# Performance work log

Measured on AMD Instinct MI355X. Metric: run time of the kernel, lower is better.

Reference implementation:

```python
import jax, jax.numpy as jnp
import numpy as np

B, C, E = 2, 128, 60000

def conv1(x, W, b):
    # pointwise conv1d: x [B,Cin,E], W [Cout,Cin], b [Cout] -> [B,Cout,E]
    return jnp.einsum('oc,bce->boe', W, x) + b[None, :, None]

def mesh_conv(x, gi, W, b):
    # MeshCNN GeMM conv: x [B,C,E], gi [B,E,4] neighbor edge ids, W [Cout,Cin,5], b [Cout]
    f = jax.vmap(lambda xb, ib: xb[:, ib])(x, gi)  # [B,C,E,4] neighbor gather
    f1, f2, f3, f4 = f[..., 0], f[..., 1], f[..., 2], f[..., 3]
    # symmetric features: [e, a+c, b+d, |a-c|, |b-d|]
    G = jnp.stack([x, f1 + f3, f2 + f4, jnp.abs(f1 - f3), jnp.abs(f2 - f4)], axis=-1)  # [B,C,E,5]
    return jnp.einsum('bces,ocs->boe', G, W) + b[None, :, None]


def setup_inputs() -> dict:
    key = jax.random.key(0)
    ks = jax.random.split(key, 16)
    s = 0.05
    return {
        'x_0': jax.random.normal(ks[0], (B, C, E), jnp.float32),
        'x_1': jax.random.normal(ks[1], (B, C, E), jnp.float32),
        'gemm': jax.random.randint(ks[2], (B, E, 4), 0, E, jnp.int32),
        'Wa_local': jax.random.normal(ks[3], (C, C), jnp.float32) * s,
        'ba_local': jax.random.normal(ks[4], (C,), jnp.float32) * s,
        'Wb_local': jax.random.normal(ks[5], (C, C), jnp.float32) * s,
        'bb_local': jax.random.normal(ks[6], (C,), jnp.float32) * s,
        'Wa_tri': jax.random.normal(ks[7], (C, C, 5), jnp.float32) * s,
        'ba_tri': jax.random.normal(ks[8], (C,), jnp.float32) * s,
        'Wb_tri': jax.random.normal(ks[9], (C, C, 5), jnp.float32) * s,
        'bb_tri': jax.random.normal(ks[10], (C,), jnp.float32) * s,
        'Wa_fuse': jax.random.normal(ks[11], (3, 2 * C), jnp.float32) * s,
        'ba_fuse': jax.random.normal(ks[12], (3,), jnp.float32) * s,
        'Wb_fuse': jax.random.normal(ks[13], (3, 2 * C), jnp.float32) * s,
        'bb_fuse': jax.random.normal(ks[14], (3,), jnp.float32) * s,
    }


def reference(x_0, x_1, gemm, Wa_local, ba_local, Wb_local, bb_local,
              Wa_tri, ba_tri, Wb_tri, bb_tri,
              Wa_fuse, ba_fuse, Wb_fuse, bb_fuse):
    a_local = conv1(x_0, Wa_local, ba_local)              # [B,C,E]
    a_tri = mesh_conv(x_0, gemm, Wa_tri, ba_tri)          # [B,C,E]
    x_a_two = jnp.concatenate([a_local, a_tri], axis=1)   # [B,2C,E]
    b_local = conv1(x_1, Wb_local, bb_local)
    b_tri = mesh_conv(x_1, gemm, Wb_tri, bb_tri)
    x_b_two = jnp.concatenate([b_local, b_tri], axis=1)
    x_a_w = conv1(x_a_two, Wa_fuse, ba_fuse)[:, None]     # [B,1,3,E]
    x_b_w = conv1(x_b_two, Wb_fuse, bb_fuse)[:, None]     # [B,1,3,E]
    return x_a_w + x_b_w
```

## Files before the change

### kernel.cpp

```cpp
#include <hip/hip_runtime.h>
#include <hip/hip_bf16.h>
#include <cstdint>

#define B_ 2
#define C_ 128
#define E_ 60000

typedef unsigned int uint32_;
typedef unsigned short ushort_;
typedef float v2f __attribute__((ext_vector_type(2)));

__device__ __forceinline__ v2f bp2(uint32_ v) {
    v2f r;
    r.x = __uint_as_float(v << 16);
    r.y = __uint_as_float(v & 0xffff0000u);
    return r;
}

__device__ __forceinline__ v2f vabs2(v2f a) {
    v2f r; r.x = fabsf(a.x); r.y = fabsf(a.y); return r;
}

__device__ __forceinline__ ushort_ f2b(float f) {
    union { float f; uint32_ u; } x; x.f = f;
    uint32_ u = x.u + 0x7fffu + ((x.u >> 16) & 1u);
    return (ushort_)(u >> 16);
}

__device__ __forceinline__ float swz_add(float v, const int pat) {
    switch (pat) {
    case 1:  return v + __int_as_float(__builtin_amdgcn_ds_swizzle(__float_as_int(v), 0x041F));
    case 2:  return v + __int_as_float(__builtin_amdgcn_ds_swizzle(__float_as_int(v), 0x081F));
    case 4:  return v + __int_as_float(__builtin_amdgcn_ds_swizzle(__float_as_int(v), 0x101F));
    case 8:  return v + __int_as_float(__builtin_amdgcn_ds_swizzle(__float_as_int(v), 0x201F));
    default: return v + __int_as_float(__builtin_amdgcn_ds_swizzle(__float_as_int(v), 0x401F));
    }
}

__global__ __launch_bounds__(256) void fuse_weights_kernel(
    const float* __restrict__ Wa_local, const float* __restrict__ ba_local,
    const float* __restrict__ Wb_local, const float* __restrict__ bb_local,
    const float* __restrict__ Wa_tri,  const float* __restrict__ ba_tri,
    const float* __restrict__ Wb_tri,  const float* __restrict__ bb_tri,
    const float* __restrict__ Wa_fuse, const float* __restrict__ ba_fuse,
    const float* __restrict__ Wb_fuse, const float* __restrict__ bb_fuse,
    float* __restrict__ Vw, float* __restrict__ cst)
{
    const int lane = threadIdx.x & 63;
    if (blockIdx.x < 15) {
        const int wid   = blockIdx.x * 4 + (threadIdx.x >> 6);
        const int pj    = wid / 10;
        const int chunk = wid % 10;
        const int p = pj / 3, j = pj % 3;
        const int f = chunk * 64 + lane;
        const float* Wf = p ? Wb_fuse : Wa_fuse;
        const float* Wt = p ? Wb_tri  : Wa_tri;
        const float* Wl = p ? Wb_local : Wa_local;
        float a0 = 0.f, a1 = 0.f, a2 = 0.f, a3 = 0.f;
        for (int o = 0; o < C_; o += 4) {
            a0 += Wf[j * 256 + 128 + o]     * Wt[(o)     * 640 + f];
            a1 += Wf[j * 256 + 128 + o + 1] * Wt[(o + 1) * 640 + f];
            a2 += Wf[j * 256 + 128 + o + 2] * Wt[(o + 2) * 640 + f];
            a3 += Wf[j * 256 + 128 + o + 3] * Wt[(o + 3) * 640 + f];
        }
        float acc = (a0 + a1) + (a2 + a3);
        const int s = f % 5, c = f / 5;
        if (s == 0) {
            float b0 = 0.f, b1 = 0.f, b2 = 0.f, b3 = 0.f;
            for (int o = 0; o < C_; o += 4) {
                b0 += Wf[j * 256 + o]     * Wl[(o)     * C_ + c];
                b1 += Wf[j * 256 + o + 1] * Wl[(o + 1) * C_ + c];
                b2 += Wf[j * 256 + o + 2] * Wl[(o + 2) * C_ + c];
                b3 += Wf[j * 256 + o + 3] * Wl[(o + 3) * C_ + c];
            }
            acc += (b0 + b1) + (b2 + b3);
        }
        Vw[(pj * 5 + s) * C_ + c] = acc;
    } else {
        if (threadIdx.x < 3) {
            int j = threadIdx.x;
            float acc = ba_fuse[j] + bb_fuse[j];
            for (int o = 0; o < C_; ++o) {
                acc += Wa_fuse[j * 256 + o]       * ba_local[o]
                     + Wa_fuse[j * 256 + 128 + o] * ba_tri[o]
                     + Wb_fuse[j * 256 + o]       * bb_local[o]
                     + Wb_fuse[j * 256 + 128 + o] * bb_tri[o];
            }
            cst[j] = acc;
        }
    }
}

__global__ __launch_bounds__(256) void transpose_bf16_kernel(
    const float* __restrict__ x0, const float* __restrict__ x1,
    ushort_* __restrict__ x0t, ushort_* __restrict__ x1t)
{
    __shared__ float tile[32][65];
    const int which = blockIdx.z >> 1;
    const int b     = blockIdx.z & 1;
    const float* src = (which ? x1 : x0) + (size_t)b * C_ * E_;
    ushort_*     dst = (which ? x1t : x0t) + (size_t)b * E_ * C_;
    const int e0 = blockIdx.x * 32;
    const int c0 = blockIdx.y * 64;
    const int t  = threadIdx.x;
    {
        const int c  = t >> 2;
        const int e8 = (t & 3) * 8;
        const float* p = src + (size_t)(c0 + c) * E_ + e0 + e8;
        float4 v0 = *(const float4*)p;
        float4 v1 = *(const float4*)(p + 4);
        tile[e8 + 0][c] = v0.x; tile[e8 + 1][c] = v0.y;
        tile[e8 + 2][c] = v0.z; tile[e8 + 3][c] = v0.w;
        tile[e8 + 4][c] = v1.x; tile[e8 + 5][c] = v1.y;
        tile[e8 + 6][c] = v1.z; tile[e8 + 7][c] = v1.w;
    }
    __syncthreads();
    {
        const int e  = t >> 3;
        const int c8 = (t & 7) * 8;
        const float* r = &tile[e][c8];
        uint32_ w0 = (uint32_)f2b(r[0]) | ((uint32_)f2b(r[1]) << 16);
        uint32_ w1 = (uint32_)f2b(r[2]) | ((uint32_)f2b(r[3]) << 16);
        uint32_ w2 = (uint32_)f2b(r[4]) | ((uint32_)f2b(r[5]) << 16);
        uint32_ w3 = (uint32_)f2b(r[6]) | ((uint32_)f2b(r[7]) << 16);
        uint4 w; w.x = w0; w.y = w1; w.z = w2; w.w = w3;
        *(uint4*)(dst + (size_t)(e0 + e) * C_ + c0 + c8) = w;
    }
}

__global__ __launch_bounds__(256, 4) void mesh_fused_kernel(
    const uint32_* __restrict__ x0t, const uint32_* __restrict__ x1t,
    const int* __restrict__ gemm, const float* __restrict__ Vw,
    const float* __restrict__ cst, float* __restrict__ out)
{
    const int lane = threadIdx.x & 63;
    const int wv   = threadIdx.x >> 6;
    const int gw   = blockIdx.x * 4 + wv;
    const int nw   = gridDim.x * 4;

    v2f w[2][3][5];
#pragma unroll
    for (int p = 0; p < 2; ++p)
#pragma unroll
        for (int j = 0; j < 3; ++j)
#pragma unroll
            for (int s = 0; s < 5; ++s)
                w[p][j][s] = *(const v2f*)(Vw + (((p * 3 + j) * 5 + s) << 7) + lane * 2);

    const int  jj     = lane >> 4;
    const bool is0    = (jj == 0), is1 = (jj == 1);
    const bool writer = ((lane & 15) == 0) && (jj < 3);
    const float cj    = is0 ? cst[0] : (is1 ? cst[1] : cst[2]);
    float* obase      = out + (size_t)(jj < 3 ? jj : 2) * E_;

    const int4* g4 = (const int4*)gemm;
    const int npair = (B_ * E_) / 2;

    int4 giA = make_int4(0, 0, 0, 0), giB = giA;
    if (gw < npair) { giA = g4[2 * gw]; giB = g4[2 * gw + 1]; }

    for (int pair = gw; pair < npair; pair += nw) {
        const int nxt = pair + nw;
        const int4 gA = giA, gB = giB;
        if (nxt < npair) { giA = g4[2 * nxt]; giB = g4[2 * nxt + 1]; }

        const int e0 = 2 * pair;
        const int b  = (e0 >= E_) ? 1 : 0;
        const int e  = e0 - (b ? E_ : 0);
        const uint32_* xa = x0t + (size_t)b * (E_ * 64);
        const uint32_* xb = x1t + (size_t)b * (E_ * 64);

        const uint32_ sA = ((uint32_)e << 6) + lane;
        const uint32_ sB = sA + 64;
        const uint32_ oA1 = ((uint32_)gA.x << 6) + lane;
        const uint32_ oA2 = ((uint32_)gA.y << 6) + lane;
        const uint32_ oA3 = ((uint32_)gA.z << 6) + lane;
        const uint32_ oA4 = ((uint32_)gA.w << 6) + lane;
        const uint32_ oB1 = ((uint32_)gB.x << 6) + lane;
        const uint32_ oB2 = ((uint32_)gB.y << 6) + lane;
        const uint32_ oB3 = ((uint32_)gB.z << 6) + lane;
        const uint32_ oB4 = ((uint32_)gB.w << 6) + lane;

        const uint32_ A0 = xa[sA],  A1 = xa[oA1], A2 = xa[oA2], A3 = xa[oA3], A4 = xa[oA4];
        const uint32_ C0 = xb[sA],  C1 = xb[oA1], C2 = xb[oA2], C3 = xb[oA3], C4 = xb[oA4];
        const uint32_ D0 = xa[sB],  D1 = xa[oB1], D2 = xa[oB2], D3 = xa[oB3], D4 = xa[oB4];
        const uint32_ F0 = xb[sB],  F1 = xb[oB1], F2 = xb[oB2], F3 = xb[oB3], F4 = xb[oB4];

        float rA0, rA1, rA2;
        {
            v2f a0 = bp2(A0), a1 = bp2(A1), a2 = bp2(A2), a3 = bp2(A3), a4 = bp2(A4);
            v2f b0 = bp2(C0), b1 = bp2(C1), b2 = bp2(C2), b3 = bp2(C3), b4 = bp2(C4);
            v2f sa1 = a1 + a3, sa2 = a2 + a4;
            v2f da1 = vabs2(a1 - a3), da2 = vabs2(a2 - a4);
            v2f sb1 = b1 + b3, sb2 = b2 + b4;
            v2f db1 = vabs2(b1 - b3), db2 = vabs2(b2 - b4);
            v2f t0 = w[0][0][0] * a0, t1 = w[0][1][0] * a0, t2 = w[0][2][0] * a0;
            t0 += w[0][0][1] * sa1; t1 += w[0][1][1] * sa1; t2 += w[0][2][1] * sa1;
            t0 += w[0][0][2] * sa2; t1 += w[0][1][2] * sa2; t2 += w[0][2][2] * sa2;
            t0 += w[0][0][3] * da1; t1 += w[0][1][3] * da1; t2 += w[0][2][3] * da1;
            t0 += w[0][0][4] * da2; t1 += w[0][1][4] * da2; t2 += w[0][2][4] * da2;
            t0 += w[1][0][0] * b0;  t1 += w[1][1][0] * b0;  t2 += w[1][2][0] * b0;
            t0 += w[1][0][1] * sb1; t1 += w[1][1][1] * sb1; t2 += w[1][2][1] * sb1;
            t0 += w[1][0][2] * sb2; t1 += w[1][1][2] * sb2; t2 += w[1][2][2] * sb2;
            t0 += w[1][0][3] * db1; t1 += w[1][1][3] * db1; t2 += w[1][2][3] * db1;
            t0 += w[1][0][4] * db2; t1 += w[1][1][4] * db2; t2 += w[1][2][4] * db2;
            rA0 = t0.x + t0.y; rA1 = t1.x + t1.y; rA2 = t2.x + t2.y;
        }
        float rB0, rB1, rB2;
        {
            v2f a0 = bp2(D0), a1 = bp2(D1), a2 = bp2(D2), a3 = bp2(D3), a4 = bp2(D4);
            v2f b0 = bp2(F0), b1 = bp2(F1), b2 = bp2(F2), b3 = bp2(F3), b4 = bp2(F4);
            v2f sa1 = a1 + a3, sa2 = a2 + a4;
            v2f da1 = vabs2(a1 - a3), da2 = vabs2(a2 - a4);
            v2f sb1 = b1 + b3, sb2 = b2 + b4;
            v2f db1 = vabs2(b1 - b3), db2 = vabs2(b2 - b4);
            v2f t0 = w[0][0][0] * a0, t1 = w[0][1][0] * a0, t2 = w[0][2][0] * a0;
            t0 += w[0][0][1] * sa1; t1 += w[0][1][1] * sa1; t2 += w[0][2][1] * sa1;
            t0 += w[0][0][2] * sa2; t1 += w[0][1][2] * sa2; t2 += w[0][2][2] * sa2;
            t0 += w[0][0][3] * da1; t1 += w[0][1][3] * da1; t2 += w[0][2][3] * da1;
            t0 += w[0][0][4] * da2; t1 += w[0][1][4] * da2; t2 += w[0][2][4] * da2;
            t0 += w[1][0][0] * b0;  t1 += w[1][1][0] * b0;  t2 += w[1][2][0] * b0;
            t0 += w[1][0][1] * sb1; t1 += w[1][1][1] * sb1; t2 += w[1][2][1] * sb1;
            t0 += w[1][0][2] * sb2; t1 += w[1][1][2] * sb2; t2 += w[1][2][2] * sb2;
            t0 += w[1][0][3] * db1; t1 += w[1][1][3] * db1; t2 += w[1][2][3] * db1;
            t0 += w[1][0][4] * db2; t1 += w[1][1][4] * db2; t2 += w[1][2][4] * db2;
            rB0 = t0.x + t0.y; rB1 = t1.x + t1.y; rB2 = t2.x + t2.y;
        }

        rA0 = swz_add(rA0, 16); rB0 = swz_add(rB0, 16);
        rA1 = swz_add(rA1, 16); rB1 = swz_add(rB1, 16);
        rA2 = swz_add(rA2, 16); rB2 = swz_add(rB2, 16);
        rA0 += __shfl_xor(rA0, 32, 64); rB0 += __shfl_xor(rB0, 32, 64);
        rA1 += __shfl_xor(rA1, 32, 64); rB1 += __shfl_xor(rB1, 32, 64);
        rA2 += __shfl_xor(rA2, 32, 64); rB2 += __shfl_xor(rB2, 32, 64);

        float vA = is0 ? rA0 : (is1 ? rA1 : rA2);
        float vB = is0 ? rB0 : (is1 ? rB1 : rB2);
        vA = swz_add(vA, 1); vB = swz_add(vB, 1);
        vA = swz_add(vA, 2); vB = swz_add(vB, 2);
        vA = swz_add(vA, 4); vB = swz_add(vB, 4);
        vA = swz_add(vA, 8); vB = swz_add(vB, 8);

        if (writer) {
            float2 st; st.x = vA + cj; st.y = vB + cj;
            *(float2*)(obase + (b ? 3 * E_ : 0) + e) = st;
        }
    }
}

extern "C" void kernel_launch(void* const* d_in, const int* in_sizes, int n_in,
                              void* d_out, int out_size, void* d_ws, size_t ws_size,
                              hipStream_t stream) {
    const float* x0       = (const float*)d_in[0];
    const float* x1       = (const float*)d_in[1];
    const int*   gemm     = (const int*)d_in[2];
    const float* Wa_local = (const float*)d_in[3];
    const float* ba_local = (const float*)d_in[4];
    const float* Wb_local = (const float*)d_in[5];
    const float* bb_local = (const float*)d_in[6];
    const float* Wa_tri   = (const float*)d_in[7];
    const float* ba_tri   = (const float*)d_in[8];
    const float* Wb_tri   = (const float*)d_in[9];
    const float* bb_tri   = (const float*)d_in[10];
    const float* Wa_fuse  = (const float*)d_in[11];
    const float* ba_fuse  = (const float*)d_in[12];
    const float* Wb_fuse  = (const float*)d_in[13];
    const float* bb_fuse  = (const float*)d_in[14];
    float* out = (float*)d_out;

    ushort_* x0t = (ushort_*)d_ws;
    ushort_* x1t = x0t + (size_t)B_ * E_ * C_;
    float*   Vw  = (float*)(x1t + (size_t)B_ * E_ * C_);
    float*   cst = Vw + 2 * 3 * 5 * C_;

    hipLaunchKernelGGL(fuse_weights_kernel, dim3(16), dim3(256), 0, stream,
                       Wa_local, ba_local, Wb_local, bb_local,
                       Wa_tri, ba_tri, Wb_tri, bb_tri,
                       Wa_fuse, ba_fuse, Wb_fuse, bb_fuse, Vw, cst);

    hipLaunchKernelGGL(transpose_bf16_kernel, dim3(E_ / 32, C_ / 64, 2 * B_),
                       dim3(256), 0, stream, x0, x1, x0t, x1t);

    hipLaunchKernelGGL(mesh_fused_kernel, dim3(2048), dim3(256), 0, stream,
                       (const uint32_*)x0t, (const uint32_*)x1t, gemm, Vw, cst, out);
}
```

Measured before the change: 227.7 us.

## Interleave x0 and x1 bf16 rows into one buffer for paired gathers

The transpose kernel now writes x0 and x1 into a single interleaved bf16 buffer, where each uint2 holds a channel pair from x0 next to the same pair from x1. The mesh kernel then gathers each neighbor edge with one 8-byte load instead of two separate 4-byte loads from two arrays. This halves the number of gather instructions and puts both inputs for an edge in the same cache lines, aiming to improve random-access efficiency. The transpose kernel uses twice the LDS per block, and its grid shrinks to one block per (b, tile) for both tensors.

After: 227.7 us. Within noise of the previous version (+0.0%).

```diff
diff --git a/kernel.cpp b/kernel.cpp
--- a/kernel.cpp
+++ b/kernel.cpp
@@ -25,6 +25,10 @@
     union { float f; uint32_ u; } x; x.f = f;
     uint32_ u = x.u + 0x7fffu + ((x.u >> 16) & 1u);
     return (ushort_)(u >> 16);
+}
+
+__device__ __forceinline__ uint32_ packb(float lo, float hi) {
+    return (uint32_)f2b(lo) | ((uint32_)f2b(hi) << 16);
 }
 
 __device__ __forceinline__ float swz_add(float v, const int pat) {
@@ -91,47 +95,57 @@
     }
 }
 
-__global__ __launch_bounds__(256) void transpose_bf16_kernel(
+__global__ __launch_bounds__(256) void transpose_interleave_kernel(
     const float* __restrict__ x0, const float* __restrict__ x1,
-    ushort_* __restrict__ x0t, ushort_* __restrict__ x1t)
+    uint32_* __restrict__ y)
 {
-    __shared__ float tile[32][65];
-    const int which = blockIdx.z >> 1;
-    const int b     = blockIdx.z & 1;
-    const float* src = (which ? x1 : x0) + (size_t)b * C_ * E_;
-    ushort_*     dst = (which ? x1t : x0t) + (size_t)b * E_ * C_;
+    __shared__ float tA[32][65];
+    __shared__ float tB[32][65];
+    const int b  = blockIdx.z;
     const int e0 = blockIdx.x * 32;
     const int c0 = blockIdx.y * 64;
-    const int t  = threadIdx.x;
+    const float* s0 = x0 + (size_t)b * C_ * E_;
+    const float* s1 = x1 + (size_t)b * C_ * E_;
+    const int t = threadIdx.x;
     {
         const int c  = t >> 2;
         const int e8 = (t & 3) * 8;
-        const float* p = src + (size_t)(c0 + c) * E_ + e0 + e8;
-        float4 v0 = *(const float4*)p;
-        float4 v1 = *(const float4*)(p + 4);
-        tile[e8 + 0][c] = v0.x; tile[e8 + 1][c] = v0.y;
-        tile[e8 + 2][c] = v0.z; tile[e8 + 3][c] = v0.w;
-        tile[e8 + 4][c] = v1.x; tile[e8 + 5][c] = v1.y;
-        tile[e8 + 6][c] = v1.z; tile[e8 + 7][c] = v1.w;
+        const float* p0 = s0 + (size_t)(c0 + c) * E_ + e0 + e8;
+        const float* p1 = s1 + (size_t)(c0 + c) * E_ + e0 + e8;
+        float4 u0 = *(const float4*)p0;
+        float4 u1 = *(const float4*)(p0 + 4);
+        float4 v0 = *(const float4*)p1;
+        float4 v1 = *(const float4*)(p1 + 4);
+        tA[e8 + 0][c] = u0.x; tA[e8 + 1][c] = u0.y;
+        tA[e8 + 2][c] = u0.z; tA[e8 + 3][c] = u0.w;
+        tA[e8 + 4][c] = u1.x; tA[e8 + 5][c] = u1.y;
+        tA[e8 + 6][c] = u1.z; tA[e8 + 7][c] = u1.w;
+        tB[e8 + 0][c] = v0.x; tB[e8 + 1][c] = v0.y;
+        tB[e8 + 2][c] = v0.z; tB[e8 + 3][c] = v0.w;
+        tB[e8 + 4][c] = v1.x; tB[e8 + 5][c] = v1.y;
+        tB[e8 + 6][c] = v1.z; tB[e8 + 7][c] = v1.w;
     }
     __syncthreads();
     {
         const int e  = t >> 3;
         const int c8 = (t & 7) * 8;
-        const float* r = &tile[e][c8];
-        uint32_ w0 = (uint32_)f2b(r[0]) | ((uint32_)f2b(r[1]) << 16);
-        uint32_ w1 = (uint32_)f2b(r[2]) | ((uint32_)f2b(r[3]) << 16);
-        uint32_ w2 = (uint32_)f2b(r[4]) | ((uint32_)f2b(r[5]) << 16);
-        uint32_ w3 = (uint32_)f2b(r[6]) | ((uint32_)f2b(r[7]) << 16);
-        uint4 w; w.x = w0; w.y = w1; w.z = w2; w.w = w3;
-        *(uint4*)(dst + (size_t)(e0 + e) * C_ + c0 + c8) = w;
+        const float* ra = &tA[e][c8];
+        const float* rb = &tB[e][c8];
+        uint4 w0, w1;
+        w0.x = packb(ra[0], ra[1]); w0.y = packb(rb[0], rb[1]);
+        w0.z = packb(ra[2], ra[3]); w0.w = packb(rb[2], rb[3]);
+        w1.x = packb(ra[4], ra[5]); w1.y = packb(rb[4], rb[5]);
+        w1.z = packb(ra[6], ra[7]); w1.w = packb(rb[6], rb[7]);
+        uint32_* drow = y + (((size_t)(b * E_ + e0 + e)) << 7) + c0 + c8;
+        *(uint4*)(drow)     = w0;
+        *(uint4*)(drow + 4) = w1;
     }
 }
 
 __global__ __launch_bounds__(256, 4) void mesh_fused_kernel(
-    const uint32_* __restrict__ x0t, const uint32_* __restrict__ x1t,
-    const int* __restrict__ gemm, const float* __restrict__ Vw,
-    const float* __restrict__ cst, float* __restrict__ out)
+    const uint2* __restrict__ y, const int* __restrict__ gemm,
+    const float* __restrict__ Vw, const float* __restrict__ cst,
+    float* __restrict__ out)
 {
     const int lane = threadIdx.x & 63;
     const int wv   = threadIdx.x >> 6;
@@ -167,11 +181,10 @@
         const int e0 = 2 * pair;
         const int b  = (e0 >= E_) ? 1 : 0;
         const int e  = e0 - (b ? E_ : 0);
-        const uint32_* xa = x0t + (size_t)b * (E_ * 64);
-        const uint32_* xb = x1t + (size_t)b * (E_ * 64);
-
-        const uint32_ sA = ((uint32_)e << 6) + lane;
-        const uint32_ sB = sA + 64;
+        const uint2* Y = y + (size_t)b * (E_ * 64);
+
+        const uint32_ sA  = ((uint32_)e    << 6) + lane;
+        const uint32_ sB  = sA + 64;
         const uint32_ oA1 = ((uint32_)gA.x << 6) + lane;
         const uint32_ oA2 = ((uint32_)gA.y << 6) + lane;
         const uint32_ oA3 = ((uint32_)gA.z << 6) + lane;
@@ -181,15 +194,17 @@
         const uint32_ oB3 = ((uint32_)gB.z << 6) + lane;
         const uint32_ oB4 = ((uint32_)gB.w << 6) + lane;
 
-        const uint32_ A0 = xa[sA],  A1 = xa[oA1], A2 = xa[oA2], A3 = xa[oA3], A4 = xa[oA4];
-        const uint32_ C0 = xb[sA],  C1 = xb[oA1], C2 = xb[oA2], C3 = xb[oA3], C4 = xb[oA4];
-        const uint32_ D0 = xa[sB],  D1 = xa[oB1], D2 = xa[oB2], D3 = xa[oB3], D4 = xa[oB4];
-        const uint32_ F0 = xb[sB],  F1 = xb[oB1], F2 = xb[oB2], F3 = xb[oB3], F4 = xb[oB4];
+        const uint2 PA0 = Y[sA],  PA1 = Y[oA1], PA2 = Y[oA2],
+                    PA3 = Y[oA3], PA4 = Y[oA4];
+        const uint2 PB0 = Y[sB],  PB1 = Y[oB1], PB2 = Y[oB2],
+                    PB3 = Y[oB3], PB4 = Y[oB4];
 
         float rA0, rA1, rA2;
         {
-            v2f a0 = bp2(A0), a1 = bp2(A1), a2 = bp2(A2), a3 = bp2(A3), a4 = bp2(A4);
-            v2f b0 = bp2(C0), b1 = bp2(C1), b2 = bp2(C2), b3 = bp2(C3), b4 = bp2(C4);
+            v2f a0 = bp2(PA0.x), a1 = bp2(PA1.x), a2 = bp2(PA2.x),
+                a3 = bp2(PA3.x), a4 = bp2(PA4.x);
+            v2f b0 = bp2(PA0.y), b1 = bp2(PA1.y), b2 = bp2(PA2.y),
+                b3 = bp2(PA3.y), b4 = bp2(PA4.y);
             v2f sa1 = a1 + a3, sa2 = a2 + a4;
             v2f da1 = vabs2(a1 - a3), da2 = vabs2(a2 - a4);
             v2f sb1 = b1 + b3, sb2 = b2 + b4;
@@ -208,8 +223,10 @@
         }
         float rB0, rB1, rB2;
         {
-            v2f a0 = bp2(D0), a1 = bp2(D1), a2 = bp2(D2), a3 = bp2(D3), a4 = bp2(D4);
-            v2f b0 = bp2(F0), b1 = bp2(F1), b2 = bp2(F2), b3 = bp2(F3), b4 = bp2(F4);
+            v2f a0 = bp2(PB0.x), a1 = bp2(PB1.x), a2 = bp2(PB2.x),
+                a3 = bp2(PB3.x), a4 = bp2(PB4.x);
+            v2f b0 = bp2(PB0.y), b1 = bp2(PB1.y), b2 = bp2(PB2.y),
+                b3 = bp2(PB3.y), b4 = bp2(PB4.y);
             v2f sa1 = a1 + a3, sa2 = a2 + a4;
             v2f da1 = vabs2(a1 - a3), da2 = vabs2(a2 - a4);
             v2f sb1 = b1 + b3, sb2 = b2 + b4;
@@ -268,9 +285,8 @@
     const float* bb_fuse  = (const float*)d_in[14];
     float* out = (float*)d_out;
 
-    ushort_* x0t = (ushort_*)d_ws;
-    ushort_* x1t = x0t + (size_t)B_ * E_ * C_;
-    float*   Vw  = (float*)(x1t + (size_t)B_ * E_ * C_);
+    uint32_* y   = (uint32_*)d_ws;
+    float*   Vw  = (float*)(y + (size_t)B_ * E_ * 128);
     float*   cst = Vw + 2 * 3 * 5 * C_;
 
     hipLaunchKernelGGL(fuse_weights_kernel, dim3(16), dim3(256), 0, stream,
@@ -278,9 +294,9 @@
                        Wa_tri, ba_tri, Wb_tri, bb_tri,
                        Wa_fuse, ba_fuse, Wb_fuse, bb_fuse, Vw, cst);
 
-    hipLaunchKernelGGL(transpose_bf16_kernel, dim3(E_ / 32, C_ / 64, 2 * B_),
-                       dim3(256), 0, stream, x0, x1, x0t, x1t);
+    hipLaunchKernelGGL(transpose_interleave_kernel, dim3(E_ / 32, C_ / 64, B_),
+                       dim3(256), 0, stream, x0, x1, y);
 
     hipLaunchKernelGGL(mesh_fused_kernel, dim3(2048), dim3(256), 0, stream,
-                       (const uint32_*)x0t, (const uint32_*)x1t, gemm, Vw, cst, out);
-}
+                       (const uint2*)y, gemm, Vw, cst, out);
+}
```

## Interleave x0/x1 bf16 layout and fold self-edge term into transpose kernel

Applied to the files above, without the earlier changes.

The transpose kernel now processes x0 and x1 together, writing one interleaved bf16 buffer so each neighbor gather fetches both inputs with a single 8-byte load. It also computes the self-edge (s=0) contribution, including the local conv, as a per-edge partial sum and writes it to a psum buffer. The mesh kernel therefore drops the self-edge loads and their FMAs, and adds psum at the write. In exchange the transpose kernel does more work and carries extra register pressure, and the design adds a small intermediate buffer plus one extra read per output.

Measured after the change: 250.0 us. 1.1x slower.

```diff
diff --git a/kernel.cpp b/kernel.cpp
--- a/kernel.cpp
+++ b/kernel.cpp
@@ -25,6 +25,10 @@
     union { float f; uint32_ u; } x; x.f = f;
     uint32_ u = x.u + 0x7fffu + ((x.u >> 16) & 1u);
     return (ushort_)(u >> 16);
+}
+
+__device__ __forceinline__ uint32_ packb(float lo, float hi) {
+    return (uint32_)f2b(lo) | ((uint32_)f2b(hi) << 16);
 }
 
 __device__ __forceinline__ float swz_add(float v, const int pat) {
@@ -44,7 +48,7 @@
     const float* __restrict__ Wb_tri,  const float* __restrict__ bb_tri,
     const float* __restrict__ Wa_fuse, const float* __restrict__ ba_fuse,
     const float* __restrict__ Wb_fuse, const float* __restrict__ bb_fuse,
-    float* __restrict__ Vw, float* __restrict__ cst)
+    float* __restrict__ Vw, float* __restrict__ Vs, float* __restrict__ cst)
 {
     const int lane = threadIdx.x & 63;
     if (blockIdx.x < 15) {
@@ -74,8 +78,10 @@
                 b3 += Wf[j * 256 + o + 3] * Wl[(o + 3) * C_ + c];
             }
             acc += (b0 + b1) + (b2 + b3);
+            Vs[pj * C_ + c] = acc;
+        } else {
+            Vw[(pj * 5 + s) * C_ + c] = acc;
         }
-        Vw[(pj * 5 + s) * C_ + c] = acc;
     } else {
         if (threadIdx.x < 3) {
             int j = threadIdx.x;
@@ -91,67 +97,131 @@
     }
 }
 
-__global__ __launch_bounds__(256) void transpose_bf16_kernel(
+__global__ __launch_bounds__(256) void transpose_fused_kernel(
     const float* __restrict__ x0, const float* __restrict__ x1,
-    ushort_* __restrict__ x0t, ushort_* __restrict__ x1t)
+    uint32_* __restrict__ y, const float* __restrict__ Vs,
+    float* __restrict__ psum)
 {
-    __shared__ float tile[32][65];
-    const int which = blockIdx.z >> 1;
-    const int b     = blockIdx.z & 1;
-    const float* src = (which ? x1 : x0) + (size_t)b * C_ * E_;
-    ushort_*     dst = (which ? x1t : x0t) + (size_t)b * E_ * C_;
-    const int e0 = blockIdx.x * 32;
-    const int c0 = blockIdx.y * 64;
-    const int t  = threadIdx.x;
+    __shared__ float tile[32][131];
+    const int b   = blockIdx.y;
+    const int e0  = blockIdx.x * 32;
+    const int t   = threadIdx.x;
+    const int c   = t >> 1;
+    const int eh  = (t & 1) * 16;
+    const int e   = t >> 3;
+    const int k16 = (t & 7) * 16;
+
+    const float* s0 = x0 + (size_t)b * C_ * E_ + (size_t)c * E_ + e0 + eh;
+    const float* s1 = x1 + (size_t)b * C_ * E_ + (size_t)c * E_ + e0 + eh;
+
+    float ra[16], rb[16];
+
     {
-        const int c  = t >> 2;
-        const int e8 = (t & 3) * 8;
-        const float* p = src + (size_t)(c0 + c) * E_ + e0 + e8;
-        float4 v0 = *(const float4*)p;
-        float4 v1 = *(const float4*)(p + 4);
-        tile[e8 + 0][c] = v0.x; tile[e8 + 1][c] = v0.y;
-        tile[e8 + 2][c] = v0.z; tile[e8 + 3][c] = v0.w;
-        tile[e8 + 4][c] = v1.x; tile[e8 + 5][c] = v1.y;
-        tile[e8 + 6][c] = v1.z; tile[e8 + 7][c] = v1.w;
-    }
+        float4 v0 = *(const float4*)(s0);
+        float4 v1 = *(const float4*)(s0 + 4);
+        float4 v2 = *(const float4*)(s0 + 8);
+        float4 v3 = *(const float4*)(s0 + 12);
+        tile[eh + 0][c] = v0.x;  tile[eh + 1][c] = v0.y;
+        tile[eh + 2][c] = v0.z;  tile[eh + 3][c] = v0.w;
+        tile[eh + 4][c] = v1.x;  tile[eh + 5][c] = v1.y;
+        tile[eh + 6][c] = v1.z;  tile[eh + 7][c] = v1.w;
+        tile[eh + 8][c] = v2.x;  tile[eh + 9][c] = v2.y;
+        tile[eh + 10][c] = v2.z; tile[eh + 11][c] = v2.w;
+        tile[eh + 12][c] = v3.x; tile[eh + 13][c] = v3.y;
+        tile[eh + 14][c] = v3.z; tile[eh + 15][c] = v3.w;
+    }
+    __syncthreads();
+#pragma unroll
+    for (int i = 0; i < 16; ++i) ra[i] = tile[e][k16 + i];
     __syncthreads();
     {
-        const int e  = t >> 3;
-        const int c8 = (t & 7) * 8;
-        const float* r = &tile[e][c8];
-        uint32_ w0 = (uint32_)f2b(r[0]) | ((uint32_)f2b(r[1]) << 16);
-        uint32_ w1 = (uint32_)f2b(r[2]) | ((uint32_)f2b(r[3]) << 16);
-        uint32_ w2 = (uint32_)f2b(r[4]) | ((uint32_)f2b(r[5]) << 16);
-        uint32_ w3 = (uint32_)f2b(r[6]) | ((uint32_)f2b(r[7]) << 16);
-        uint4 w; w.x = w0; w.y = w1; w.z = w2; w.w = w3;
-        *(uint4*)(dst + (size_t)(e0 + e) * C_ + c0 + c8) = w;
-    }
-}
+        float4 v0 = *(const float4*)(s1);
+        float4 v1 = *(const float4*)(s1 + 4);
+        float4 v2 = *(const float4*)(s1 + 8);
+        float4 v3 = *(const float4*)(s1 + 12);
+        tile[eh + 0][c] = v0.x;  tile[eh + 1][c] = v0.y;
+        tile[eh + 2][c] = v0.z;  tile[eh + 3][c] = v0.w;
+        tile[eh + 4][c] = v1.x;  tile[eh + 5][c] = v1.y;
+        tile[eh + 6][c] = v1.z;  tile[eh + 7][c] = v1.w;
+        tile[eh + 8][c] = v2.x;  tile[eh + 9][c] = v2.y;
+        tile[eh + 10][c] = v2.z; tile[eh + 11][c] = v2.w;
+        tile[eh + 12][c] = v3.x; tile[eh + 13][c] = v3.y;
+        tile[eh + 14][c] = v3.z; tile[eh + 15][c] = v3.w;
+    }
+    __syncthreads();
+#pragma unroll
+    for (int i = 0; i < 16; ++i) rb[i] = tile[e][k16 + i];
+
+    uint32_* drow = y + (((size_t)(b * E_ + e0 + e)) << 7) + k16;
+#pragma unroll
+    for (int m = 0; m < 4; ++m) {
+        uint4 w_;
+        w_.x = packb(ra[4 * m],     ra[4 * m + 1]);
+        w_.y = packb(rb[4 * m],     rb[4 * m + 1]);
+        w_.z = packb(ra[4 * m + 2], ra[4 * m + 3]);
+        w_.w = packb(rb[4 * m + 2], rb[4 * m + 3]);
+        *(uint4*)(drow + 4 * m) = w_;
+    }
+
+    float p0 = 0.f, p1 = 0.f, p2 = 0.f;
+#pragma unroll
+    for (int i = 0; i < 16; ++i) {
+        const float va = ra[i], vb = rb[i];
+        p0 += Vs[0 * C_ + k16 + i] * va + Vs[3 * C_ + k16 + i] * vb;
+        p1 += Vs[1 * C_ + k16 + i] * va + Vs[4 * C_ + k16 + i] * vb;
+        p2 += Vs[2 * C_ + k16 + i] * va + Vs[5 * C_ + k16 + i] * vb;
+    }
+    p0 = swz_add(p0, 1); p0 = swz_add(p0, 2); p0 = swz_add(p0, 4);
+    p1 = swz_add(p1, 1); p1 = swz_add(p1, 2); p1 = swz_add(p1, 4);
+    p2 = swz_add(p2, 1); p2 = swz_add(p2, 2); p2 = swz_add(p2, 4);
+    const int m = t & 7;
+    if (m < 3) {
+        float v = (m == 0) ? p0 : ((m == 1) ? p1 : p2);
+        psum[((size_t)b * 3 + m) * E_ + e0 + e] = v;
+    }
+}
+
+#define LDW(p, j, s) (*(const v2f*)(Vw + ((((p) * 3 + (j)) * 5 + (s)) << 7) + (lane << 1)))
+
+#define EDGE_DOT(P1,P2,P3,P4, R0,R1,R2) do {                                  \
+    v2f a1 = bp2(P1.x), a2 = bp2(P2.x), a3 = bp2(P3.x), a4 = bp2(P4.x);       \
+    v2f b1 = bp2(P1.y), b2 = bp2(P2.y), b3 = bp2(P3.y), b4 = bp2(P4.y);       \
+    v2f sa1 = a1 + a3, sa2 = a2 + a4;                                         \
+    v2f da1 = vabs2(a1 - a3), da2 = vabs2(a2 - a4);                           \
+    v2f sb1 = b1 + b3, sb2 = b2 + b4;                                         \
+    v2f db1 = vabs2(b1 - b3), db2 = vabs2(b2 - b4);                           \
+    v2f t0 = w001 * sa1 + w002 * sa2 + w003 * da1 + w004 * da2                \
+           + w101 * sb1 + w102 * sb2 + w103 * db1 + w104 * db2;               \
+    v2f t1 = w011 * sa1 + w012 * sa2 + w013 * da1 + w014 * da2                \
+           + w111 * sb1 + w112 * sb2 + w113 * db1 + w114 * db2;               \
+    v2f t2 = w021 * sa1 + w022 * sa2 + w023 * da1 + w024 * da2                \
+           + w121 * sb1 + w122 * sb2 + w123 * db1 + w124 * db2;               \
+    R0 = t0.x + t0.y; R1 = t1.x + t1.y; R2 = t2.x + t2.y;                     \
+} while (0)
 
 __global__ __launch_bounds__(256, 4) void mesh_fused_kernel(
-    const uint32_* __restrict__ x0t, const uint32_* __restrict__ x1t,
-    const int* __restrict__ gemm, const float* __restrict__ Vw,
-    const float* __restrict__ cst, float* __restrict__ out)
+    const uint2* __restrict__ yy, const int* __restrict__ gemm,
+    const float* __restrict__ Vw, const float* __restrict__ cst,
+    const float* __restrict__ psum, float* __restrict__ out)
 {
     const int lane = threadIdx.x & 63;
     const int wv   = threadIdx.x >> 6;
     const int gw   = blockIdx.x * 4 + wv;
     const int nw   = gridDim.x * 4;
 
-    v2f w[2][3][5];
-#pragma unroll
-    for (int p = 0; p < 2; ++p)
-#pragma unroll
-        for (int j = 0; j < 3; ++j)
-#pragma unroll
-            for (int s = 0; s < 5; ++s)
-                w[p][j][s] = *(const v2f*)(Vw + (((p * 3 + j) * 5 + s) << 7) + lane * 2);
+    v2f w001 = LDW(0,0,1), w002 = LDW(0,0,2), w003 = LDW(0,0,3), w004 = LDW(0,0,4);
+    v2f w011 = LDW(0,1,1), w012 = LDW(0,1,2), w013 = LDW(0,1,3), w014 = LDW(0,1,4);
+    v2f w021 = LDW(0,2,1), w022 = LDW(0,2,2), w023 = LDW(0,2,3), w024 = LDW(0,2,4);
+    v2f w101 = LDW(1,0,1), w102 = LDW(1,0,2), w103 = LDW(1,0,3), w104 = LDW(1,0,4);
+    v2f w111 = LDW(1,1,1), w112 = LDW(1,1,2), w113 = LDW(1,1,3), w114 = LDW(1,1,4);
+    v2f w121 = LDW(1,2,1), w122 = LDW(1,2,2), w123 = LDW(1,2,3), w124 = LDW(1,2,4);
 
     const int  jj     = lane >> 4;
     const bool is0    = (jj == 0), is1 = (jj == 1);
     const bool writer = ((lane & 15) == 0) && (jj < 3);
     const float cj    = is0 ? cst[0] : (is1 ? cst[1] : cst[2]);
     float* obase      = out + (size_t)(jj < 3 ? jj : 2) * E_;
+    const float* pbase = psum + (size_t)(jj < 3 ? jj : 2) * E_;
 
     const int4* g4 = (const int4*)gemm;
     const int npair = (B_ * E_) / 2;
@@ -167,11 +237,8 @@
         const int e0 = 2 * pair;
         const int b  = (e0 >= E_) ? 1 : 0;
         const int e  = e0 - (b ? E_ : 0);
-        const uint32_* xa = x0t + (size_t)b * (E_ * 64);
-        const uint32_* xb = x1t + (size_t)b * (E_ * 64);
-
-        const uint32_ sA = ((uint32_)e << 6) + lane;
-        const uint32_ sB = sA + 64;
+        const uint2* Y = yy + (size_t)b * (E_ * 64);
+
         const uint32_ oA1 = ((uint32_)gA.x << 6) + lane;
         const uint32_ oA2 = ((uint32_)gA.y << 6) + lane;
         const uint32_ oA3 = ((uint32_)gA.z << 6) + lane;
@@ -181,51 +248,12 @@
         const uint32_ oB3 = ((uint32_)gB.z << 6) + lane;
         const uint32_ oB4 = ((uint32_)gB.w << 6) + lane;
 
-        const uint32_ A0 = xa[sA],  A1 = xa[oA1], A2 = xa[oA2], A3 = xa[oA3], A4 = xa[oA4];
-        const uint32_ C0 = xb[sA],  C1 = xb[oA1], C2 = xb[oA2], C3 = xb[oA3], C4 = xb[oA4];
-        const uint32_ D0 = xa[sB],  D1 = xa[oB1], D2 = xa[oB2], D3 = xa[oB3], D4 = xa[oB4];
-        const uint32_ F0 = xb[sB],  F1 = xb[oB1], F2 = xb[oB2], F3 = xb[oB3], F4 = xb[oB4];
-
-        float rA0, rA1, rA2;
-        {
-            v2f a0 = bp2(A0), a1 = bp2(A1), a2 = bp2(A2), a3 = bp2(A3), a4 = bp2(A4);
-            v2f b0 = bp2(C0), b1 = bp2(C1), b2 = bp2(C2), b3 = bp2(C3), b4 = bp2(C4);
-            v2f sa1 = a1 + a3, sa2 = a2 + a4;
-            v2f da1 = vabs2(a1 - a3), da2 = vabs2(a2 - a4);
-            v2f sb1 = b1 + b3, sb2 = b2 + b4;
-            v2f db1 = vabs2(b1 - b3), db2 = vabs2(b2 - b4);
-            v2f t0 = w[0][0][0] * a0, t1 = w[0][1][0] * a0, t2 = w[0][2][0] * a0;
-            t0 += w[0][0][1] * sa1; t1 += w[0][1][1] * sa1; t2 += w[0][2][1] * sa1;
-            t0 += w[0][0][2] * sa2; t1 += w[0][1][2] * sa2; t2 += w[0][2][2] * sa2;
-            t0 += w[0][0][3] * da1; t1 += w[0][1][3] * da1; t2 += w[0][2][3] * da1;
-            t0 += w[0][0][4] * da2; t1 += w[0][1][4] * da2; t2 += w[0][2][4] * da2;
-            t0 += w[1][0][0] * b0;  t1 += w[1][1][0] * b0;  t2 += w[1][2][0] * b0;
-            t0 += w[1][0][1] * sb1; t1 += w[1][1][1] * sb1; t2 += w[1][2][1] * sb1;
-            t0 += w[1][0][2] * sb2; t1 += w[1][1][2] * sb2; t2 += w[1][2][2] * sb2;
-            t0 += w[1][0][3] * db1; t1 += w[1][1][3] * db1; t2 += w[1][2][3] * db1;
-            t0 += w[1][0][4] * db2; t1 += w[1][1][4] * db2; t2 += w[1][2][4] * db2;
-            rA0 = t0.x + t0.y; rA1 = t1.x + t1.y; rA2 = t2.x + t2.y;
-        }
-        float rB0, rB1, rB2;
-        {
-            v2f a0 = bp2(D0), a1 = bp2(D1), a2 = bp2(D2), a3 = bp2(D3), a4 = bp2(D4);
-            v2f b0 = bp2(F0), b1 = bp2(F1), b2 = bp2(F2), b3 = bp2(F3), b4 = bp2(F4);
-            v2f sa1 = a1 + a3, sa2 = a2 + a4;
-            v2f da1 = vabs2(a1 - a3), da2 = vabs2(a2 - a4);
-            v2f sb1 = b1 + b3, sb2 = b2 + b4;
-            v2f db1 = vabs2(b1 - b3), db2 = vabs2(b2 - b4);
-            v2f t0 = w[0][0][0] * a0, t1 = w[0][1][0] * a0, t2 = w[0][2][0] * a0;
-            t0 += w[0][0][1] * sa1; t1 += w[0][1][1] * sa1; t2 += w[0][2][1] * sa1;
-            t0 += w[0][0][2] * sa2; t1 += w[0][1][2] * sa2; t2 += w[0][2][2] * sa2;
-            t0 += w[0][0][3] * da1; t1 += w[0][1][3] * da1; t2 += w[0][2][3] * da1;
-            t0 += w[0][0][4] * da2; t1 += w[0][1][4] * da2; t2 += w[0][2][4] * da2;
-            t0 += w[1][0][0] * b0;  t1 += w[1][1][0] * b0;  t2 += w[1][2][0] * b0;
-            t0 += w[1][0][1] * sb1; t1 += w[1][1][1] * sb1; t2 += w[1][2][1] * sb1;
-            t0 += w[1][0][2] * sb2; t1 += w[1][1][2] * sb2; t2 += w[1][2][2] * sb2;
-            t0 += w[1][0][3] * db1; t1 += w[1][1][3] * db1; t2 += w[1][2][3] * db1;
-            t0 += w[1][0][4] * db2; t1 += w[1][1][4] * db2; t2 += w[1][2][4] * db2;
-            rB0 = t0.x + t0.y; rB1 = t1.x + t1.y; rB2 = t2.x + t2.y;
-        }
+        const uint2 PA1 = Y[oA1], PA2 = Y[oA2], PA3 = Y[oA3], PA4 = Y[oA4];
+        const uint2 PB1 = Y[oB1], PB2 = Y[oB2], PB3 = Y[oB3], PB4 = Y[oB4];
+
+        float rA0, rA1, rA2, rB0, rB1, rB2;
+        EDGE_DOT(PA1, PA2, PA3, PA4, rA0, rA1, rA2);
+        EDGE_DOT(PB1, PB2, PB3, PB4, rB0, rB1, rB2);
 
         rA0 = swz_add(rA0, 16); rB0 = swz_add(rB0, 16);
         rA1 = swz_add(rA1, 16); rB1 = swz_add(rB1, 16);
@@ -242,8 +270,11 @@
         vA = swz_add(vA, 8); vB = swz_add(vB, 8);
 
         if (writer) {
-            float2 st; st.x = vA + cj; st.y = vB + cj;
-            *(float2*)(obase + (b ? 3 * E_ : 0) + e) = st;
+            const float2 ps = *(const float2*)(pbase + (size_t)b * 3 * E_ + e);
+            float2 st;
+            st.x = vA + cj + ps.x;
+            st.y = vB + cj + ps.y;
+            *(float2*)(obase + (size_t)b * 3 * E_ + e) = st;
         }
     }
 }
@@ -268,19 +299,20 @@
     const float* bb_fuse  = (const float*)d_in[14];
     float* out = (float*)d_out;
 
-    ushort_* x0t = (ushort_*)d_ws;
-    ushort_* x1t = x0t + (size_t)B_ * E_ * C_;
-    float*   Vw  = (float*)(x1t + (size_t)B_ * E_ * C_);
-    float*   cst = Vw + 2 * 3 * 5 * C_;
+    uint32_* y    = (uint32_*)d_ws;
+    float*   psum = (float*)(y + (size_t)B_ * E_ * 128);
+    float*   Vw   = psum + (size_t)B_ * 3 * E_;
+    float*   Vs   = Vw + 2 * 3 * 5 * C_;
+    float*   cst  = Vs + 6 * C_;
 
     hipLaunchKernelGGL(fuse_weights_kernel, dim3(16), dim3(256), 0, stream,
                        Wa_local, ba_local, Wb_local, bb_local,
                        Wa_tri, ba_tri, Wb_tri, bb_tri,
-                       Wa_fuse, ba_fuse, Wb_fuse, bb_fuse, Vw, cst);
-
-    hipLaunchKernelGGL(transpose_bf16_kernel, dim3(E_ / 32, C_ / 64, 2 * B_),
-                       dim3(256), 0, stream, x0, x1, x0t, x1t);
+                       Wa_fuse, ba_fuse, Wb_fuse, bb_fuse, Vw, Vs, cst);
+
+    hipLaunchKernelGGL(transpose_fused_kernel, dim3(E_ / 32, B_),
+                       dim3(256), 0, stream, x0, x1, y, Vs, psum);
 
     hipLaunchKernelGGL(mesh_fused_kernel, dim3(2048), dim3(256), 0, stream,
-                       (const uint32_*)x0t, (const uint32_*)x1t, gemm, Vw, cst, out);
-}
+                       (const uint2*)y, gemm, Vw, cst, psum, out);
+}
```
